# Kernel tuning notes

Hardware: AMD Instinct MI355X
Metric: run time of the kernel (lower is better)

## Reference

```python
import jax, jax.numpy as jnp
import numpy as np

POOL_SIZE = 7  # matches init kwarg pool_size


def setup_inputs() -> dict:
    key = jax.random.key(0)
    k1, k2 = jax.random.split(key, 2)
    H, W, C, N = 50, 64, 1024, 1000
    stride = 16
    shared_layers = jax.random.normal(k1, (1, H, W, C), dtype=jnp.float32)
    # ROIs in image coordinates (y1, x1, y2, x2), image ~ (H*stride, W*stride)
    img_h, img_w = float(H * stride), float(W * stride)
    u = jax.random.uniform(k2, (N, 4), dtype=jnp.float32)
    y1 = u[:, 0] * (img_h * 0.6)
    x1 = u[:, 1] * (img_w * 0.6)
    y2 = y1 + 32.0 + u[:, 2] * (img_h * 0.4 - 32.0)
    x2 = x1 + 32.0 + u[:, 3] * (img_w * 0.4 - 32.0)
    rois = jnp.stack([y1, x1, y2, x2], axis=1)
    return {"shared_layers": shared_layers, "rois": rois, "extractor_stride": stride}


def _crop_and_resize(img, boxes, cs):
    """TF tf.image.crop_and_resize (bilinear, extrapolation_value=0) for a single image.
    img: [H, W, C]; boxes: [N, 4] normalized (y1, x1, y2, x2); cs: crop size (>1).
    Returns [N, cs, cs, C]."""
    H, W, C = img.shape
    y1, x1, y2, x2 = boxes[:, 0], boxes[:, 1], boxes[:, 2], boxes[:, 3]
    i = jnp.arange(cs, dtype=boxes.dtype)
    # sample coordinates in source pixel space: [N, cs]
    ys = y1[:, None] * (H - 1) + i[None, :] * ((y2 - y1) * (H - 1) / (cs - 1))[:, None]
    xs = x1[:, None] * (W - 1) + i[None, :] * ((x2 - x1) * (W - 1) / (cs - 1))[:, None]
    valid_y = (ys >= 0) & (ys <= H - 1)
    valid_x = (xs >= 0) & (xs <= W - 1)
    y0f = jnp.floor(ys)
    x0f = jnp.floor(xs)
    wy = (ys - y0f)[:, :, None, None]   # [N, cs, 1, 1]
    wx = (xs - x0f)[:, None, :, None]   # [N, 1, cs, 1]
    y0 = jnp.clip(y0f.astype(jnp.int32), 0, H - 1)
    y1i = jnp.clip(y0 + 1, 0, H - 1)
    x0 = jnp.clip(x0f.astype(jnp.int32), 0, W - 1)
    x1i = jnp.clip(x0 + 1, 0, W - 1)

    def gather(yi, xi):  # -> [N, cs, cs, C]
        return img[yi[:, :, None], xi[:, None, :]]

    top = gather(y0, x0) * (1.0 - wx) + gather(y0, x1i) * wx
    bot = gather(y1i, x0) * (1.0 - wx) + gather(y1i, x1i) * wx
    out = top * (1.0 - wy) + bot * wy
    mask = (valid_y[:, :, None] & valid_x[:, None, :])[..., None]
    return jnp.where(mask, out, jnp.zeros((), dtype=img.dtype))


def reference(shared_layers, rois, extractor_stride):
    rois = rois / jnp.asarray(extractor_stride, dtype=rois.dtype)
    H, W = shared_layers.shape[1], shared_layers.shape[2]
    # normalize (y1/h, x1/w, y2/h, x2/w)
    boxes = rois / jnp.array([H, W, H, W], dtype=rois.dtype)
    cs = POOL_SIZE * 2  # pre_pool_size
    crops = _crop_and_resize(shared_layers[0], boxes, cs)  # [N, 14, 14, C]
    N, C = crops.shape[0], crops.shape[-1]
    # MaxPooling2D pool 2x2 stride 2 (14 even -> padding irrelevant)
    pooled = crops.reshape(N, POOL_SIZE, 2, POOL_SIZE, 2, C).max(axis=(2, 4))
    return jax.lax.stop_gradient(pooled.reshape(N, -1))
```

## Files before the change

### kernel.cpp

```cpp
#include <hip/hip_runtime.h>
#include <math.h>

namespace {

constexpr int kRowF4 = 64 * 256;

typedef float vf4 __attribute__((ext_vector_type(4)));

__device__ __forceinline__ int rfl(int x) { return __builtin_amdgcn_readfirstlane(x); }
__device__ __forceinline__ float rflf(float x) {
  union { float f; int i; } u;
  u.f = x;
  u.i = __builtin_amdgcn_readfirstlane(u.i);
  return u.f;
}

__device__ __forceinline__ vf4 splat4(float x) {
  vf4 v = {x, x, x, x};
  return v;
}

__global__ __launch_bounds__(256) void roi_pool_kernel(
    const float* __restrict__ img,
    const float* __restrict__ rois,
    const int* __restrict__ stride_p,
    float* __restrict__ out) {
  const int bid = blockIdx.x;
  const int chunk = gridDim.x >> 3;
  const int pos = ((gridDim.x & 7) == 0) ? ((bid & 7) * chunk + (bid >> 3)) : bid;
  const int n  = pos / 49;
  const int rr = pos - n * 49;
  const int py = rr / 7;
  const int px = rr - py * 7;
  const int c4 = threadIdx.x;

  const float s = (float)(*stride_p);
  const float by1 = rois[n * 4 + 0] / s / 50.0f;
  const float bx1 = rois[n * 4 + 1] / s / 64.0f;
  const float by2 = rois[n * 4 + 2] / s / 50.0f;
  const float bx2 = rois[n * 4 + 3] / s / 64.0f;
  const float stepy = (by2 - by1) * 49.0f / 13.0f;
  const float stepx = (bx2 - bx1) * 63.0f / 13.0f;

  const float ys0 = by1 * 49.0f + (float)(2 * py + 0) * stepy;
  const float ys1 = by1 * 49.0f + (float)(2 * py + 1) * stepy;
  const float xs0 = bx1 * 63.0f + (float)(2 * px + 0) * stepx;
  const float xs1 = bx1 * 63.0f + (float)(2 * px + 1) * stepx;

  const float vy0 = (ys0 >= 0.0f && ys0 <= 49.0f) ? 1.0f : 0.0f;
  const float vy1 = (ys1 >= 0.0f && ys1 <= 49.0f) ? 1.0f : 0.0f;
  const float vx0 = (xs0 >= 0.0f && xs0 <= 63.0f) ? 1.0f : 0.0f;
  const float vx1 = (xs1 >= 0.0f && xs1 <= 63.0f) ? 1.0f : 0.0f;

  const float yf0 = floorf(ys0), yf1 = floorf(ys1);
  const float xf0 = floorf(xs0), xf1 = floorf(xs1);
  const float wy0 = ys0 - yf0, wy1 = ys1 - yf1;
  const float wx0 = xs0 - xf0, wx1 = xs1 - xf1;

  const int r0i = min(max((int)yf0, 0), 49);
  const int r2i = min(max((int)yf1, 0), 49);
  const int c0i = min(max((int)xf0, 0), 63);
  const int c2i = min(max((int)xf1, 0), 63);
  const int r0 = rfl(r0i);
  const int r1 = rfl(min(r0i + 1, 49));
  const int r2 = rfl(r2i);
  const int r3 = rfl(min(r2i + 1, 49));
  const int c0 = rfl(c0i);
  const int c1 = rfl(min(c0i + 1, 63));
  const int c2 = rfl(c2i);
  const int c3 = rfl(min(c2i + 1, 63));

  const vf4 gy0 = splat4(rflf((1.0f - wy0) * vy0));
  const vf4 fy0 = splat4(rflf(wy0 * vy0));
  const vf4 gy1 = splat4(rflf((1.0f - wy1) * vy1));
  const vf4 fy1 = splat4(rflf(wy1 * vy1));
  const vf4 gx0 = splat4(rflf((1.0f - wx0) * vx0));
  const vf4 fx0 = splat4(rflf(wx0 * vx0));
  const vf4 gx1 = splat4(rflf((1.0f - wx1) * vx1));
  const vf4 fx1 = splat4(rflf(wx1 * vx1));

  const vf4* __restrict__ img4 = (const vf4*)img;

  const bool c2e0 = (c2 == c0), c2e1 = (c2 == c1);
  const bool c3e1 = (c3 == c1), c3e2 = (c3 == c2);
  const int co0 = c0 * 256, co1 = c1 * 256, co2 = c2 * 256, co3 = c3 * 256;

  auto rowblend = [&](int r, vf4& b0, vf4& b1) {
    const vf4* rp = img4 + r * kRowF4;
    const vf4 q0 = rp[co0 + c4];
    const vf4 q1 = rp[co1 + c4];
    vf4 q2, q3;
    if (c2e0)      q2 = q0;
    else if (c2e1) q2 = q1;
    else           q2 = rp[co2 + c4];
    if (c3e1)      q3 = q1;
    else if (c3e2) q3 = q2;
    else           q3 = rp[co3 + c4];
    b0 = q0 * gx0 + q1 * fx0;
    b1 = q2 * gx1 + q3 * fx1;
  };

  vf4 b00, b01, b10, b11, b20, b21, b30, b31;
  rowblend(r0, b00, b01);
  if (r1 == r0) { b10 = b00; b11 = b01; }
  else rowblend(r1, b10, b11);
  if (r2 == r0)      { b20 = b00; b21 = b01; }
  else if (r2 == r1) { b20 = b10; b21 = b11; }
  else rowblend(r2, b20, b21);
  if (r3 == r1)      { b30 = b10; b31 = b11; }
  else if (r3 == r2) { b30 = b20; b31 = b21; }
  else rowblend(r3, b30, b31);

  vf4 m = b00 * gy0 + b10 * fy0;
  vf4 v = b01 * gy0 + b11 * fy0;
  m = __builtin_elementwise_max(m, v);
  v = b20 * gy1 + b30 * fy1;
  m = __builtin_elementwise_max(m, v);
  v = b21 * gy1 + b31 * fy1;
  m = __builtin_elementwise_max(m, v);

  __builtin_nontemporal_store(m, (vf4*)out + (size_t)pos * 256 + c4);
}

}

extern "C" void kernel_launch(void* const* d_in, const int* in_sizes, int n_in,
                              void* d_out, int out_size, void* d_ws, size_t ws_size,
                              hipStream_t stream) {
  const float* img      = (const float*)d_in[0];
  const float* rois     = (const float*)d_in[1];
  const int*   stride_p = (const int*)d_in[2];
  float*       out      = (float*)d_out;

  const int N = in_sizes[1] / 4;
  const int nblocks = N * 49;
  roi_pool_kernel<<<nblocks, 256, 0, stream>>>(img, rois, stride_p, out);
}
```

Before: 107.3 us.

## Precompute per-ROI sample row/column offsets and weights in a setup kernel

Adds a small setup kernel that computes, for each ROI and pooled row or column, the clamped source byte offsets and validity-masked bilinear weights, and writes them to a workspace table. The main pooling kernel then loads these from the table instead of recomputing divisions, floors and clamps in every block. This trims scalar setup work per block but adds a second launch and a dependent table load at the start of each block. The original kernel is kept as a fallback when the workspace is too small.

```diff
diff --git a/kernel.cpp b/kernel.cpp
--- a/kernel.cpp
+++ b/kernel.cpp
@@ -3,27 +3,69 @@
 
 namespace {
 
-constexpr int kRowF4 = 64 * 256;
-
 typedef float vf4 __attribute__((ext_vector_type(4)));
 
+constexpr int kRowBytes = 64 * 1024 * 4;
+constexpr int kColBytes = 1024 * 4;
+
 __device__ __forceinline__ int rfl(int x) { return __builtin_amdgcn_readfirstlane(x); }
-__device__ __forceinline__ float rflf(float x) {
-  union { float f; int i; } u;
-  u.f = x;
-  u.i = __builtin_amdgcn_readfirstlane(u.i);
-  return u.f;
-}
 
 __device__ __forceinline__ vf4 splat4(float x) {
   vf4 v = {x, x, x, x};
   return v;
 }
 
-__global__ __launch_bounds__(256) void roi_pool_kernel(
+__global__ void roi_setup_kernel(const float* __restrict__ rois,
+                                 const int* __restrict__ stride_p,
+                                 int4* __restrict__ tab, int N) {
+  const int t = blockIdx.x * 64 + threadIdx.x;
+  if (t >= N * 7) return;
+  const int n = t / 7;
+  const int k = t - n * 7;
+
+  const float s = (float)(*stride_p);
+  const float by1 = rois[n * 4 + 0] / s / 50.0f;
+  const float bx1 = rois[n * 4 + 1] / s / 64.0f;
+  const float by2 = rois[n * 4 + 2] / s / 50.0f;
+  const float bx2 = rois[n * 4 + 3] / s / 64.0f;
+  const float stepy = (by2 - by1) * 49.0f / 13.0f;
+  const float stepx = (bx2 - bx1) * 63.0f / 13.0f;
+
+  const float ys0 = by1 * 49.0f + (float)(2 * k + 0) * stepy;
+  const float ys1 = by1 * 49.0f + (float)(2 * k + 1) * stepy;
+  const float vy0 = (ys0 >= 0.0f && ys0 <= 49.0f) ? 1.0f : 0.0f;
+  const float vy1 = (ys1 >= 0.0f && ys1 <= 49.0f) ? 1.0f : 0.0f;
+  const float yf0 = floorf(ys0), yf1 = floorf(ys1);
+  const float wy0 = ys0 - yf0, wy1 = ys1 - yf1;
+  const int r0 = min(max((int)yf0, 0), 49);
+  const int r1 = min(r0 + 1, 49);
+  const int r2 = min(max((int)yf1, 0), 49);
+  const int r3 = min(r2 + 1, 49);
+  tab[2 * t] = make_int4(r0 * kRowBytes, r1 * kRowBytes,
+                         r2 * kRowBytes, r3 * kRowBytes);
+  ((float4*)tab)[2 * t + 1] =
+      make_float4((1.0f - wy0) * vy0, wy0 * vy0, (1.0f - wy1) * vy1, wy1 * vy1);
+
+  const float xs0 = bx1 * 63.0f + (float)(2 * k + 0) * stepx;
+  const float xs1 = bx1 * 63.0f + (float)(2 * k + 1) * stepx;
+  const float vx0 = (xs0 >= 0.0f && xs0 <= 63.0f) ? 1.0f : 0.0f;
+  const float vx1 = (xs1 >= 0.0f && xs1 <= 63.0f) ? 1.0f : 0.0f;
+  const float xf0 = floorf(xs0), xf1 = floorf(xs1);
+  const float wx0 = xs0 - xf0, wx1 = xs1 - xf1;
+  const int c0 = min(max((int)xf0, 0), 63);
+  const int c1 = min(c0 + 1, 63);
+  const int c2 = min(max((int)xf1, 0), 63);
+  const int c3 = min(c2 + 1, 63);
+  const int xoff = N * 14;
+  tab[xoff + 2 * t] = make_int4(c0 * kColBytes, c1 * kColBytes,
+                                c2 * kColBytes, c3 * kColBytes);
+  ((float4*)tab)[xoff + 2 * t + 1] =
+      make_float4((1.0f - wx0) * vx0, wx0 * vx0, (1.0f - wx1) * vx1, wx1 * vx1);
+}
+
+__global__ __launch_bounds__(256) void roi_pool_tab(
     const float* __restrict__ img,
-    const float* __restrict__ rois,
-    const int* __restrict__ stride_p,
+    const int4* __restrict__ tab, int N,
     float* __restrict__ out) {
   const int bid = blockIdx.x;
   const int chunk = gridDim.x >> 3;
@@ -34,6 +76,82 @@
   const int px = rr - py * 7;
   const int c4 = threadIdx.x;
 
+  const int yt = 2 * (n * 7 + py);
+  const int xt = N * 14 + 2 * (n * 7 + px);
+  const int4   yi = tab[yt];
+  const float4 yw = ((const float4*)tab)[yt + 1];
+  const int4   xi = tab[xt];
+  const float4 xw = ((const float4*)tab)[xt + 1];
+
+  const int r0 = rfl(yi.x), r1 = rfl(yi.y), r2 = rfl(yi.z), r3 = rfl(yi.w);
+  const int c0 = rfl(xi.x), c1 = rfl(xi.y), c2 = rfl(xi.z), c3 = rfl(xi.w);
+
+  const vf4 gy0 = splat4(yw.x), fy0 = splat4(yw.y);
+  const vf4 gy1 = splat4(yw.z), fy1 = splat4(yw.w);
+  const vf4 gx0 = splat4(xw.x), fx0 = splat4(xw.y);
+  const vf4 gx1 = splat4(xw.z), fx1 = splat4(xw.w);
+
+  const char* __restrict__ imgb = (const char*)img;
+  const int coff = c4 * 16;
+
+  const bool c2e0 = (c2 == c0), c2e1 = (c2 == c1);
+  const bool c3e1 = (c3 == c1), c3e2 = (c3 == c2);
+
+  auto rowblend = [&](int rB, vf4& b0, vf4& b1) {
+    const vf4 q0 = *(const vf4*)(imgb + (rB + c0) + coff);
+    const vf4 q1 = *(const vf4*)(imgb + (rB + c1) + coff);
+    vf4 q2, q3;
+    if (c2e0)      q2 = q0;
+    else if (c2e1) q2 = q1;
+    else           q2 = *(const vf4*)(imgb + (rB + c2) + coff);
+    if (c3e1)      q3 = q1;
+    else if (c3e2) q3 = q2;
+    else           q3 = *(const vf4*)(imgb + (rB + c3) + coff);
+    b0 = q0 * gx0 + q1 * fx0;
+    b1 = q2 * gx1 + q3 * fx1;
+  };
+
+  vf4 b00, b01, b10, b11, b20, b21, b30, b31;
+  rowblend(r0, b00, b01);
+  if (r1 == r0) { b10 = b00; b11 = b01; }
+  else rowblend(r1, b10, b11);
+  if (r2 == r0)      { b20 = b00; b21 = b01; }
+  else if (r2 == r1) { b20 = b10; b21 = b11; }
+  else rowblend(r2, b20, b21);
+  if (r3 == r1)      { b30 = b10; b31 = b11; }
+  else if (r3 == r2) { b30 = b20; b31 = b21; }
+  else rowblend(r3, b30, b31);
+
+  vf4 m = b00 * gy0 + b10 * fy0;
+  vf4 v = b01 * gy0 + b11 * fy0;
+  m = __builtin_elementwise_max(m, v);
+  v = b20 * gy1 + b30 * fy1;
+  m = __builtin_elementwise_max(m, v);
+  v = b21 * gy1 + b31 * fy1;
+  m = __builtin_elementwise_max(m, v);
+
+  __builtin_nontemporal_store(m, (vf4*)out + (size_t)pos * 256 + c4);
+}
+
+__device__ __forceinline__ float rflf(float x) {
+  union { float f; int i; } u;
+  u.f = x;
+  u.i = __builtin_amdgcn_readfirstlane(u.i);
+  return u.f;
+}
+
+__global__ __launch_bounds__(256) void roi_pool_kernel(
+    const float* __restrict__ img, const float* __restrict__ rois,
+    const int* __restrict__ stride_p, float* __restrict__ out) {
+  const int bid = blockIdx.x;
+  const int chunk = gridDim.x >> 3;
+  const int pos = ((gridDim.x & 7) == 0) ? ((bid & 7) * chunk + (bid >> 3)) : bid;
+  const int n  = pos / 49;
+  const int rr = pos - n * 49;
+  const int py = rr / 7;
+  const int px = rr - py * 7;
+  const int c4 = threadIdx.x;
+
   const float s = (float)(*stride_p);
   const float by1 = rois[n * 4 + 0] / s / 50.0f;
   const float bx1 = rois[n * 4 + 1] / s / 64.0f;
@@ -46,30 +164,22 @@
   const float ys1 = by1 * 49.0f + (float)(2 * py + 1) * stepy;
   const float xs0 = bx1 * 63.0f + (float)(2 * px + 0) * stepx;
   const float xs1 = bx1 * 63.0f + (float)(2 * px + 1) * stepx;
-
   const float vy0 = (ys0 >= 0.0f && ys0 <= 49.0f) ? 1.0f : 0.0f;
   const float vy1 = (ys1 >= 0.0f && ys1 <= 49.0f) ? 1.0f : 0.0f;
   const float vx0 = (xs0 >= 0.0f && xs0 <= 63.0f) ? 1.0f : 0.0f;
   const float vx1 = (xs1 >= 0.0f && xs1 <= 63.0f) ? 1.0f : 0.0f;
-
   const float yf0 = floorf(ys0), yf1 = floorf(ys1);
   const float xf0 = floorf(xs0), xf1 = floorf(xs1);
   const float wy0 = ys0 - yf0, wy1 = ys1 - yf1;
   const float wx0 = xs0 - xf0, wx1 = xs1 - xf1;
-
   const int r0i = min(max((int)yf0, 0), 49);
   const int r2i = min(max((int)yf1, 0), 49);
   const int c0i = min(max((int)xf0, 0), 63);
   const int c2i = min(max((int)xf1, 0), 63);
-  const int r0 = rfl(r0i);
-  const int r1 = rfl(min(r0i + 1, 49));
-  const int r2 = rfl(r2i);
-  const int r3 = rfl(min(r2i + 1, 49));
-  const int c0 = rfl(c0i);
-  const int c1 = rfl(min(c0i + 1, 63));
-  const int c2 = rfl(c2i);
-  const int c3 = rfl(min(c2i + 1, 63));
-
+  const int r0 = rfl(r0i), r1 = rfl(min(r0i + 1, 49));
+  const int r2 = rfl(r2i), r3 = rfl(min(r2i + 1, 49));
+  const int c0 = rfl(c0i), c1 = rfl(min(c0i + 1, 63));
+  const int c2 = rfl(c2i), c3 = rfl(min(c2i + 1, 63));
   const vf4 gy0 = splat4(rflf((1.0f - wy0) * vy0));
   const vf4 fy0 = splat4(rflf(wy0 * vy0));
   const vf4 gy1 = splat4(rflf((1.0f - wy1) * vy1));
@@ -80,13 +190,12 @@
   const vf4 fx1 = splat4(rflf(wx1 * vx1));
 
   const vf4* __restrict__ img4 = (const vf4*)img;
-
   const bool c2e0 = (c2 == c0), c2e1 = (c2 == c1);
   const bool c3e1 = (c3 == c1), c3e2 = (c3 == c2);
   const int co0 = c0 * 256, co1 = c1 * 256, co2 = c2 * 256, co3 = c3 * 256;
 
   auto rowblend = [&](int r, vf4& b0, vf4& b1) {
-    const vf4* rp = img4 + r * kRowF4;
+    const vf4* rp = img4 + r * (64 * 256);
     const vf4 q0 = rp[co0 + c4];
     const vf4 q1 = rp[co1 + c4];
     vf4 q2, q3;
@@ -133,6 +242,14 @@
   float*       out      = (float*)d_out;
 
   const int N = in_sizes[1] / 4;
-  const int nblocks = N * 49;
-  roi_pool_kernel<<<nblocks, 256, 0, stream>>>(img, rois, stride_p, out);
-}
+  const size_t tab_bytes = (size_t)N * 28 * 16;
+
+  if (ws_size >= tab_bytes) {
+    int4* tab = (int4*)d_ws;
+    const int nt = N * 7;
+    roi_setup_kernel<<<(nt + 63) / 64, 64, 0, stream>>>(rois, stride_p, tab, N);
+    roi_pool_tab<<<N * 49, 256, 0, stream>>>(img, tab, N, out);
+  } else {
+    roi_pool_kernel<<<N * 49, 256, 0, stream>>>(img, rois, stride_p, out);
+  }
+}
```

New measurement: 98.80 us. 7.9% less time.
